# Kernel tuning notes

Hardware: AMD Instinct MI355X
Metric: run time of the kernel (lower is better)

## Reference

```python
import jax, jax.numpy as jnp
import numpy as np

NUM_ITER = 3  # num_itterations

def squash(s):
    # Faithful to the module's (non-standard) squash: out = |s|^2 * s / (1 + |s|^2 * (|s| + 1e-9)).
    # torch sums over dim=-2 of [..., D, 1]; here s is [..., D] so sum over last axis.
    sq = jnp.sum(s * s, axis=-1, keepdims=True)
    norm = jnp.sqrt(sq)
    return sq * s / (1.0 + sq * (norm + 1e-9))

def setup_inputs() -> dict:
    key = jax.random.key(0)
    k1, k2 = jax.random.split(key)
    B, P, N, T, D = 512, 1152, 10, 16, 8
    x = jax.random.normal(k1, (B, P, D), dtype=jnp.float32)          # input capsules
    W = jax.random.normal(k2, (P, N, T, D), dtype=jnp.float32)       # routing transform (torch W with leading 1 dropped)
    return {"x": x, "W": W}

def reference(x, B_unused=None, *, _=None, **__):
    raise RuntimeError('placeholder')

def reference(x, W):
    # prediction u_hat[b,p,n,:] = W[p,n] @ x[b,p]  -> [B, P, N, T]
    pred = jnp.einsum('pntd,bpd->bpnt', W, x)
    B, P, N = pred.shape[0], pred.shape[1], pred.shape[2]
    b_ij = jnp.zeros((B, P, N), dtype=x.dtype)
    v = None
    for i in range(NUM_ITER):
        # torch.tensor(c_ij) detaches the coupling coefficients from the graph
        c = jax.lax.stop_gradient(jax.nn.softmax(b_ij, axis=2))      # softmax over next-caps dim
        s = jnp.einsum('bpn,bpnt->bnt', c, pred)                     # weighted sum over prev caps
        v = squash(s)                                                # [B, N, T]
        if i < NUM_ITER - 1:
            a = jnp.einsum('bpnt,bnt->bpn', pred, v)                 # agreement
            b_ij = b_ij + jnp.mean(a, axis=0, keepdims=True)         # torch mean over batch, keepdim, broadcast-add
    return v[..., None]  # [B, numNextCaps, nextCapsDim, 1] matching torch v_j.squeeze(1)
```

## Files before the change

kernel.cpp:

```cpp
#include <hip/hip_runtime.h>
#include <hip/hip_bf16.h>


typedef __attribute__((ext_vector_type(8))) short bfrag;
typedef __attribute__((ext_vector_type(4))) float f32x4;

constexpr int B_ = 512, P_ = 1152, N_ = 10, NT_ = 160;
constexpr int K1_ = 9216, NKC_ = 288;

__device__ __forceinline__ unsigned short f2bf(float f) {
    unsigned u = __float_as_uint(f);
    return (unsigned short)((u + 0x7fffu + ((u >> 16) & 1u)) >> 16);
}
__device__ __forceinline__ float bf2f(unsigned short s) {
    return __uint_as_float((unsigned)s << 16);
}
__device__ __forceinline__ bfrag mkfrag(f32x4 a, f32x4 b, float c) {
    bfrag f;
    f[0] = (short)f2bf(a.x * c); f[1] = (short)f2bf(a.y * c);
    f[2] = (short)f2bf(a.z * c); f[3] = (short)f2bf(a.w * c);
    f[4] = (short)f2bf(b.x * c); f[5] = (short)f2bf(b.y * c);
    f[6] = (short)f2bf(b.z * c); f[7] = (short)f2bf(b.w * c);
    return f;
}

__global__ __launch_bounds__(256) void k_prep(const float* __restrict__ x,
                                              const float* __restrict__ W,
                                              unsigned short* __restrict__ Xb,
                                              unsigned short* __restrict__ Xga,
                                              unsigned short* __restrict__ Wc,
                                              unsigned short* __restrict__ Wb) {
    const int bid = blockIdx.x, tid = threadIdx.x;
    const int w = tid >> 6, ln = tid & 63, col = ln & 15, q = ln >> 4;
    if (bid < 1152) {
        __shared__ unsigned short tile[64][72];
        const int pd0 = (bid >> 3) * 64, b0 = (bid & 7) * 64;
        const int c0 = tid & 63, r0 = tid >> 6;
#pragma unroll
        for (int i = 0; i < 16; ++i) {
            const int br = i * 4 + r0;
            tile[c0][br] = f2bf(x[(size_t)(b0 + br) * K1_ + pd0 + c0]);
        }
        __syncthreads();
#pragma unroll
        for (int fi = 0; fi < 2; ++fi) {
            const int f = w + fi * 4;
            const int pdblk_l = f & 3, kc_l = f >> 2;
            bfrag fr;
#pragma unroll
            for (int j = 0; j < 8; ++j)
                fr[j] = (short)tile[pdblk_l * 16 + col][kc_l * 32 + q * 8 + j];
            const size_t addr = ((size_t)(((pd0 >> 4) + pdblk_l) * 16 + (b0 >> 5) + kc_l)) * 512 + ln * 8;
            *(bfrag*)(Xga + addr) = fr;
        }
#pragma unroll
        for (int fi = 0; fi < 2; ++fi) {
            const int f = w + fi * 4;
            const int mblk_l = f & 3, kc_l = f >> 2;
            bfrag fr;
#pragma unroll
            for (int j = 0; j < 8; ++j)
                fr[j] = (short)tile[kc_l * 32 + q * 8 + j][mblk_l * 16 + col];
            const size_t addr = ((size_t)(((b0 >> 4) + mblk_l) * NKC_ + (pd0 >> 5) + kc_l)) * 512 + ln * 8;
            *(bfrag*)(Xb + addr) = fr;
        }
    } else if (bid < 1872) {
        const int task = (bid - 1152) * 4 + w;
        const int n = task / NKC_, kc = task % NKC_;
        const int p = kc * 4 + q;
        const float* wr = W + ((size_t)p * NT_ + n * 16 + col) * 8;
        const bfrag f = mkfrag(*(const f32x4*)wr, *(const f32x4*)(wr + 4), 0.1f);
        *(bfrag*)(Wc + ((size_t)(n * NKC_ + kc)) * 512 + ln * 8) = f;
    } else {
        const int idx = (bid - 1872) * 256 + tid;
        const int p = ((idx >> 6) * 16 + (idx & 15)) >> 3, d = idx & 7;
        const int q2 = (idx & 63) >> 4;
        unsigned short* dst = Wb + (size_t)idx * 40;
#pragma unroll
        for (int mt = 0; mt < N_; ++mt)
#pragma unroll
            for (int r = 0; r < 4; ++r)
                dst[mt * 4 + r] = f2bf(W[((size_t)p * NT_ + mt * 16 + q2 * 4 + r) * 8 + d]);
    }
}

__global__ __launch_bounds__(1024) void k_sv(const unsigned short* __restrict__ Xb,
                                             const unsigned short* __restrict__ Wc,
                                             unsigned short* __restrict__ Vt,
                                             float* __restrict__ outp,
                                             int final_it) {
    __shared__ float red[16][2][256];
    const int tid = threadIdx.x;
    const int w = tid >> 6, lane = tid & 63, col = lane & 15, q = lane >> 4;
    const int mblk = blockIdx.x;
    const int n0 = blockIdx.y * 2;

    f32x4 accA = (f32x4){0.f, 0.f, 0.f, 0.f};
    f32x4 accB = (f32x4){0.f, 0.f, 0.f, 0.f};
    const int kc0 = w * 18;
    const unsigned short* Xp = Xb + ((size_t)(mblk * NKC_ + kc0)) * 512 + lane * 8;
    const unsigned short* W0 = Wc + ((size_t)(n0 * NKC_ + kc0)) * 512 + lane * 8;
    const unsigned short* W1 = W0 + (size_t)NKC_ * 512;
#pragma unroll 3
    for (int i = 0; i < 18; ++i) {
        const bfrag a  = *(const bfrag*)Xp;
        const bfrag b0 = *(const bfrag*)W0;
        const bfrag b1 = *(const bfrag*)W1;
        accA = __builtin_amdgcn_mfma_f32_16x16x32_bf16(a, b0, accA, 0, 0, 0);
        accB = __builtin_amdgcn_mfma_f32_16x16x32_bf16(a, b1, accB, 0, 0, 0);
        Xp += 512; W0 += 512; W1 += 512;
    }
#pragma unroll
    for (int r = 0; r < 4; ++r) {
        red[w][0][r * 64 + q * 16 + col] = accA[r];
        red[w][1][r * 64 + q * 16 + col] = accB[r];
    }
    __syncthreads();
    if (w < 2) {
        const int mt = n0 + w;
#pragma unroll
        for (int r = 0; r < 4; ++r) {
            const int li = r * 64 + q * 16 + col;
            float s = 0.f;
#pragma unroll
            for (int j = 0; j < 16; ++j) s += red[j][w][li];
            float sq = s * s;
            sq += __shfl_xor(sq, 1);
            sq += __shfl_xor(sq, 2);
            sq += __shfl_xor(sq, 4);
            sq += __shfl_xor(sq, 8);
            const float norm = sqrtf(sq);
            const float scale = sq / (1.0f + sq * (norm + 1e-9f));
            const float vv = s * scale;
            const int b = mblk * 16 + q * 4 + r;
            if (final_it) {
                outp[(size_t)b * NT_ + mt * 16 + col] = vv;
            } else {
                const int b5 = b & 31;
                Vt[((size_t)((mblk >> 1) * N_ + mt)) * 512
                   + ((b5 >> 3) * 16 + col) * 8 + (b5 & 7)] = f2bf(vv);
            }
        }
    }
}

__global__ __launch_bounds__(512) void k_ga(const unsigned short* __restrict__ Vt,
                                            const unsigned short* __restrict__ Xga,
                                            const unsigned short* __restrict__ Wb,
                                            const float* __restrict__ W,
                                            float* __restrict__ bbar,
                                            unsigned short* __restrict__ Wc,
                                            int accum) {
    __shared__ float bred[2][3][64][41];
    __shared__ float csm[4][N_];
    const int tid = threadIdx.x;
    const int w = tid >> 6, lane = tid & 63, col = lane & 15, q = lane >> 4;
    const int half = w >> 2, wl = w & 3;
    const int pdblk = blockIdx.x * 2 + half;
    const int p = (pdblk * 16 + col) >> 3, d = col & 7;

    f32x4 acc[N_];
#pragma unroll
    for (int mt = 0; mt < N_; ++mt) acc[mt] = (f32x4){0.f, 0.f, 0.f, 0.f};

    const int kb0 = wl * 4;
#pragma unroll
    for (int kc = kb0; kc < kb0 + 4; ++kc) {
        const bfrag bf = *(const bfrag*)(Xga + ((size_t)(pdblk * 16 + kc)) * 512 + lane * 8);
#pragma unroll
        for (int mt = 0; mt < N_; ++mt) {
            const bfrag af = *(const bfrag*)(Vt + ((size_t)(kc * N_ + mt)) * 512 + lane * 8);
            acc[mt] = __builtin_amdgcn_mfma_f32_16x16x32_bf16(af, bf, acc[mt], 0, 0, 0);
        }
    }
    if (wl) {
#pragma unroll
        for (int mt = 0; mt < N_; ++mt)
#pragma unroll
            for (int r = 0; r < 4; ++r)
                bred[half][wl - 1][lane][mt * 4 + r] = acc[mt][r];
    }
    __syncthreads();
    if (wl == 0) {
        unsigned short wv[40];
        const unsigned short* ws2 = Wb + ((size_t)(pdblk * 64 + lane)) * 40;
#pragma unroll
        for (int v = 0; v < 40; ++v) wv[v] = ws2[v];
        float part[N_];
#pragma unroll
        for (int mt = 0; mt < N_; ++mt) {
            float s = 0.f;
#pragma unroll
            for (int r = 0; r < 4; ++r) {
                const float h = acc[mt][r] + bred[half][0][lane][mt * 4 + r]
                              + bred[half][1][lane][mt * 4 + r]
                              + bred[half][2][lane][mt * 4 + r];
                s = fmaf(bf2f(wv[mt * 4 + r]), h, s);
            }
            s += __shfl_xor(s, 1);
            s += __shfl_xor(s, 2);
            s += __shfl_xor(s, 4);
            s += __shfl_xor(s, 16);
            s += __shfl_xor(s, 32);
            part[mt] = s;
        }
        if (q == 0 && d == 0) {
            const int pl = col >> 3;
            float bv[N_];
#pragma unroll
            for (int mt = 0; mt < N_; ++mt) {
                bv[mt] = part[mt] * (1.0f / 512.0f);
                if (accum) bv[mt] += bbar[(size_t)p * N_ + mt];
                bbar[(size_t)p * N_ + mt] = bv[mt];
            }
            float m = -1e30f;
#pragma unroll
            for (int mt = 0; mt < N_; ++mt) m = fmaxf(m, bv[mt]);
            float sum = 0.f;
#pragma unroll
            for (int mt = 0; mt < N_; ++mt) { bv[mt] = __expf(bv[mt] - m); sum += bv[mt]; }
            const float inv = 1.f / sum;
#pragma unroll
            for (int mt = 0; mt < N_; ++mt) csm[half * 2 + pl][mt] = bv[mt] * inv;
        }
    }
    __syncthreads();
    const int p0 = blockIdx.x * 4;
#pragma unroll
    for (int task = tid; task < 640; task += 512) {
        const int pl = task / 160, rem = task % 160;
        const int n = rem >> 4, cl = rem & 15;
        const int pp = p0 + pl;
        const float c = csm[pl][n];
        const float* wr = W + ((size_t)pp * NT_ + n * 16 + cl) * 8;
        const size_t addr = ((size_t)(n * NKC_ + (pp >> 2))) * 512 + (pp & 3) * 128 + cl * 8;
        *(bfrag*)(Wc + addr) = mkfrag(*(const f32x4*)wr, *(const f32x4*)(wr + 4), c);
    }
}

extern "C" void kernel_launch(void* const* d_in, const int* in_sizes, int n_in,
                              void* d_out, int out_size, void* d_ws, size_t ws_size,
                              hipStream_t stream) {
    const float* x = (const float*)d_in[0];
    const float* W = (const float*)d_in[1];

    char* wsp = (char*)d_ws;
    float* bbar = (float*)wsp;
    unsigned short* Xb  = (unsigned short*)(wsp + 46080);
    unsigned short* Xga = Xb + (size_t)32 * NKC_ * 512;
    unsigned short* Wc  = Xga + (size_t)576 * 16 * 512;
    unsigned short* Wb  = Wc + (size_t)N_ * NKC_ * 512;
    unsigned short* Vt  = Wb + (size_t)576 * 64 * 40;
    float* outp = (float*)d_out;

    k_prep<<<dim3(2016), dim3(256), 0, stream>>>(x, W, Xb, Xga, Wc, Wb);
    k_sv<<<dim3(32, 5), dim3(1024), 0, stream>>>(Xb, Wc, Vt, outp, 0);
    k_ga<<<dim3(288), dim3(512), 0, stream>>>(Vt, Xga, Wb, W, bbar, Wc, 0);
    k_sv<<<dim3(32, 5), dim3(1024), 0, stream>>>(Xb, Wc, Vt, outp, 0);
    k_ga<<<dim3(288), dim3(512), 0, stream>>>(Vt, Xga, Wb, W, bbar, Wc, 1);
    k_sv<<<dim3(32, 5), dim3(1024), 0, stream>>>(Xb, Wc, Vt, outp, 1);
}
```

Baseline: 136.1 us.

## Register-tile k_sv over two batch tiles and widen k_ga blocks to 1024 threads

```diff
diff --git a/kernel.cpp b/kernel.cpp
--- a/kernel.cpp
+++ b/kernel.cpp
@@ -89,35 +89,45 @@
                                              unsigned short* __restrict__ Vt,
                                              float* __restrict__ outp,
                                              int final_it) {
-    __shared__ float red[16][2][256];
+    __shared__ float red[16][4][256];
     const int tid = threadIdx.x;
     const int w = tid >> 6, lane = tid & 63, col = lane & 15, q = lane >> 4;
-    const int mblk = blockIdx.x;
+    const int bx = blockIdx.x;
     const int n0 = blockIdx.y * 2;
 
-    f32x4 accA = (f32x4){0.f, 0.f, 0.f, 0.f};
-    f32x4 accB = (f32x4){0.f, 0.f, 0.f, 0.f};
+    f32x4 acc00 = (f32x4){0.f, 0.f, 0.f, 0.f};
+    f32x4 acc01 = (f32x4){0.f, 0.f, 0.f, 0.f};
+    f32x4 acc10 = (f32x4){0.f, 0.f, 0.f, 0.f};
+    f32x4 acc11 = (f32x4){0.f, 0.f, 0.f, 0.f};
     const int kc0 = w * 18;
-    const unsigned short* Xp = Xb + ((size_t)(mblk * NKC_ + kc0)) * 512 + lane * 8;
+    const unsigned short* X0 = Xb + ((size_t)((2 * bx) * NKC_ + kc0)) * 512 + lane * 8;
+    const unsigned short* X1 = X0 + (size_t)NKC_ * 512;
     const unsigned short* W0 = Wc + ((size_t)(n0 * NKC_ + kc0)) * 512 + lane * 8;
     const unsigned short* W1 = W0 + (size_t)NKC_ * 512;
 #pragma unroll 3
     for (int i = 0; i < 18; ++i) {
-        const bfrag a  = *(const bfrag*)Xp;
+        const bfrag a0 = *(const bfrag*)X0;
+        const bfrag a1 = *(const bfrag*)X1;
         const bfrag b0 = *(const bfrag*)W0;
         const bfrag b1 = *(const bfrag*)W1;
-        accA = __builtin_amdgcn_mfma_f32_16x16x32_bf16(a, b0, accA, 0, 0, 0);
-        accB = __builtin_amdgcn_mfma_f32_16x16x32_bf16(a, b1, accB, 0, 0, 0);
-        Xp += 512; W0 += 512; W1 += 512;
+        acc00 = __builtin_amdgcn_mfma_f32_16x16x32_bf16(a0, b0, acc00, 0, 0, 0);
+        acc01 = __builtin_amdgcn_mfma_f32_16x16x32_bf16(a0, b1, acc01, 0, 0, 0);
+        acc10 = __builtin_amdgcn_mfma_f32_16x16x32_bf16(a1, b0, acc10, 0, 0, 0);
+        acc11 = __builtin_amdgcn_mfma_f32_16x16x32_bf16(a1, b1, acc11, 0, 0, 0);
+        X0 += 512; X1 += 512; W0 += 512; W1 += 512;
     }
 #pragma unroll
     for (int r = 0; r < 4; ++r) {
-        red[w][0][r * 64 + q * 16 + col] = accA[r];
-        red[w][1][r * 64 + q * 16 + col] = accB[r];
+        const int li = r * 64 + q * 16 + col;
+        red[w][0][li] = acc00[r];
+        red[w][1][li] = acc01[r];
+        red[w][2][li] = acc10[r];
+        red[w][3][li] = acc11[r];
     }
     __syncthreads();
-    if (w < 2) {
-        const int mt = n0 + w;
+    if (w < 4) {
+        const int mi = w >> 1, ni = w & 1;
+        const int mt = n0 + ni;
 #pragma unroll
         for (int r = 0; r < 4; ++r) {
             const int li = r * 64 + q * 16 + col;
@@ -132,31 +142,31 @@
             const float norm = sqrtf(sq);
             const float scale = sq / (1.0f + sq * (norm + 1e-9f));
             const float vv = s * scale;
-            const int b = mblk * 16 + q * 4 + r;
+            const int b = (2 * bx + mi) * 16 + q * 4 + r;
             if (final_it) {
                 outp[(size_t)b * NT_ + mt * 16 + col] = vv;
             } else {
                 const int b5 = b & 31;
-                Vt[((size_t)((mblk >> 1) * N_ + mt)) * 512
+                Vt[((size_t)(bx * N_ + mt)) * 512
                    + ((b5 >> 3) * 16 + col) * 8 + (b5 & 7)] = f2bf(vv);
             }
         }
     }
 }
 
-__global__ __launch_bounds__(512) void k_ga(const unsigned short* __restrict__ Vt,
-                                            const unsigned short* __restrict__ Xga,
-                                            const unsigned short* __restrict__ Wb,
-                                            const float* __restrict__ W,
-                                            float* __restrict__ bbar,
-                                            unsigned short* __restrict__ Wc,
-                                            int accum) {
-    __shared__ float bred[2][3][64][41];
-    __shared__ float csm[4][N_];
+__global__ __launch_bounds__(1024) void k_ga(const unsigned short* __restrict__ Vt,
+                                             const unsigned short* __restrict__ Xga,
+                                             const unsigned short* __restrict__ Wb,
+                                             const float* __restrict__ W,
+                                             float* __restrict__ bbar,
+                                             unsigned short* __restrict__ Wc,
+                                             int accum) {
+    __shared__ float bred[4][3][64][41];
+    __shared__ float csm[8][N_];
     const int tid = threadIdx.x;
     const int w = tid >> 6, lane = tid & 63, col = lane & 15, q = lane >> 4;
-    const int half = w >> 2, wl = w & 3;
-    const int pdblk = blockIdx.x * 2 + half;
+    const int qt = w >> 2, wl = w & 3;
+    const int pdblk = blockIdx.x * 4 + qt;
     const int p = (pdblk * 16 + col) >> 3, d = col & 7;
 
     f32x4 acc[N_];
@@ -178,7 +188,7 @@
         for (int mt = 0; mt < N_; ++mt)
 #pragma unroll
             for (int r = 0; r < 4; ++r)
-                bred[half][wl - 1][lane][mt * 4 + r] = acc[mt][r];
+                bred[qt][wl - 1][lane][mt * 4 + r] = acc[mt][r];
     }
     __syncthreads();
     if (wl == 0) {
@@ -192,9 +202,9 @@
             float s = 0.f;
 #pragma unroll
             for (int r = 0; r < 4; ++r) {
-                const float h = acc[mt][r] + bred[half][0][lane][mt * 4 + r]
-                              + bred[half][1][lane][mt * 4 + r]
-                              + bred[half][2][lane][mt * 4 + r];
+                const float h = acc[mt][r] + bred[qt][0][lane][mt * 4 + r]
+                              + bred[qt][1][lane][mt * 4 + r]
+                              + bred[qt][2][lane][mt * 4 + r];
                 s = fmaf(bf2f(wv[mt * 4 + r]), h, s);
             }
             s += __shfl_xor(s, 1);
@@ -221,13 +231,13 @@
             for (int mt = 0; mt < N_; ++mt) { bv[mt] = __expf(bv[mt] - m); sum += bv[mt]; }
             const float inv = 1.f / sum;
 #pragma unroll
-            for (int mt = 0; mt < N_; ++mt) csm[half * 2 + pl][mt] = bv[mt] * inv;
+            for (int mt = 0; mt < N_; ++mt) csm[qt * 2 + pl][mt] = bv[mt] * inv;
         }
     }
     __syncthreads();
-    const int p0 = blockIdx.x * 4;
-#pragma unroll
-    for (int task = tid; task < 640; task += 512) {
+    const int p0 = blockIdx.x * 8;
+#pragma unroll
+    for (int task = tid; task < 1280; task += 1024) {
         const int pl = task / 160, rem = task % 160;
         const int n = rem >> 4, cl = rem & 15;
         const int pp = p0 + pl;
@@ -254,9 +264,9 @@
     float* outp = (float*)d_out;
 
     k_prep<<<dim3(2016), dim3(256), 0, stream>>>(x, W, Xb, Xga, Wc, Wb);
-    k_sv<<<dim3(32, 5), dim3(1024), 0, stream>>>(Xb, Wc, Vt, outp, 0);
-    k_ga<<<dim3(288), dim3(512), 0, stream>>>(Vt, Xga, Wb, W, bbar, Wc, 0);
-    k_sv<<<dim3(32, 5), dim3(1024), 0, stream>>>(Xb, Wc, Vt, outp, 0);
-    k_ga<<<dim3(288), dim3(512), 0, stream>>>(Vt, Xga, Wb, W, bbar, Wc, 1);
-    k_sv<<<dim3(32, 5), dim3(1024), 0, stream>>>(Xb, Wc, Vt, outp, 1);
-}
+    k_sv<<<dim3(16, 5), dim3(1024), 0, stream>>>(Xb, Wc, Vt, outp, 0);
+    k_ga<<<dim3(144), dim3(1024), 0, stream>>>(Vt, Xga, Wb, W, bbar, Wc, 0);
+    k_sv<<<dim3(16, 5), dim3(1024), 0, stream>>>(Xb, Wc, Vt, outp, 0);
+    k_ga<<<dim3(144), dim3(1024), 0, stream>>>(Vt, Xga, Wb, W, bbar, Wc, 1);
+    k_sv<<<dim3(16, 5), dim3(1024), 0, stream>>>(Xb, Wc, Vt, outp, 1);
+}
```

Result: slower. 146.1 us (+7.3%).

## Stage W through shared memory in prep and widen k_ga blocks to three pd-blocks

Applied to the files above, without the earlier changes.

```diff
diff --git a/kernel.cpp b/kernel.cpp
--- a/kernel.cpp
+++ b/kernel.cpp
@@ -30,11 +30,43 @@
                                               unsigned short* __restrict__ Xga,
                                               unsigned short* __restrict__ Wc,
                                               unsigned short* __restrict__ Wb) {
+    __shared__ float smem[5760];
     const int bid = blockIdx.x, tid = threadIdx.x;
     const int w = tid >> 6, ln = tid & 63, col = ln & 15, q = ln >> 4;
-    if (bid < 1152) {
-        __shared__ unsigned short tile[64][72];
-        const int pd0 = (bid >> 3) * 64, b0 = (bid & 7) * 64;
+    if (bid < 288) {
+        const int pb = bid;
+        const int p0 = pb * 4;
+#pragma unroll
+        for (int k = 0; k < 20; ++k) {
+            const int e = k * 256 + tid;
+            const int pl = e / 1280, rem = e % 1280;
+            const int row = rem >> 3, d = rem & 7;
+            smem[pl * 1440 + row * 9 + d] = W[(size_t)p0 * 1280 + e];
+        }
+        __syncthreads();
+        for (int n = w; n < N_; n += 4) {
+            const float* src = smem + q * 1440 + (n * 16 + col) * 9;
+            bfrag f;
+#pragma unroll
+            for (int j = 0; j < 8; ++j) f[j] = (short)f2bf(src[j] * 0.1f);
+            *(bfrag*)(Wc + ((size_t)(n * NKC_ + pb)) * 512 + ln * 8) = f;
+        }
+        if (tid < 128) {
+            const int pdblk_l = tid >> 6;
+            const int lane = tid & 63, c2 = lane & 15, q2 = lane >> 4;
+            const int p_l = (pdblk_l * 16 + c2) >> 3, d = c2 & 7;
+            const float* src = smem + p_l * 1440 + d;
+            unsigned short* dst = Wb + ((size_t)((2 * pb + pdblk_l) * 64 + lane)) * 40;
+#pragma unroll
+            for (int mt = 0; mt < N_; ++mt)
+#pragma unroll
+                for (int r = 0; r < 4; ++r)
+                    dst[mt * 4 + r] = f2bf(src[(mt * 16 + q2 * 4 + r) * 9]);
+        }
+    } else {
+        unsigned short (*tile)[72] = (unsigned short (*)[72])smem;
+        const int tb = bid - 288;
+        const int pd0 = (tb >> 3) * 64, b0 = (tb & 7) * 64;
         const int c0 = tid & 63, r0 = tid >> 6;
 #pragma unroll
         for (int i = 0; i < 16; ++i) {
@@ -64,23 +96,6 @@
             const size_t addr = ((size_t)(((b0 >> 4) + mblk_l) * NKC_ + (pd0 >> 5) + kc_l)) * 512 + ln * 8;
             *(bfrag*)(Xb + addr) = fr;
         }
-    } else if (bid < 1872) {
-        const int task = (bid - 1152) * 4 + w;
-        const int n = task / NKC_, kc = task % NKC_;
-        const int p = kc * 4 + q;
-        const float* wr = W + ((size_t)p * NT_ + n * 16 + col) * 8;
-        const bfrag f = mkfrag(*(const f32x4*)wr, *(const f32x4*)(wr + 4), 0.1f);
-        *(bfrag*)(Wc + ((size_t)(n * NKC_ + kc)) * 512 + ln * 8) = f;
-    } else {
-        const int idx = (bid - 1872) * 256 + tid;
-        const int p = ((idx >> 6) * 16 + (idx & 15)) >> 3, d = idx & 7;
-        const int q2 = (idx & 63) >> 4;
-        unsigned short* dst = Wb + (size_t)idx * 40;
-#pragma unroll
-        for (int mt = 0; mt < N_; ++mt)
-#pragma unroll
-            for (int r = 0; r < 4; ++r)
-                dst[mt * 4 + r] = f2bf(W[((size_t)p * NT_ + mt * 16 + q2 * 4 + r) * 8 + d]);
     }
 }
 
@@ -144,19 +159,19 @@
     }
 }
 
-__global__ __launch_bounds__(512) void k_ga(const unsigned short* __restrict__ Vt,
+__global__ __launch_bounds__(768) void k_ga(const unsigned short* __restrict__ Vt,
                                             const unsigned short* __restrict__ Xga,
                                             const unsigned short* __restrict__ Wb,
                                             const float* __restrict__ W,
                                             float* __restrict__ bbar,
                                             unsigned short* __restrict__ Wc,
                                             int accum) {
-    __shared__ float bred[2][3][64][41];
-    __shared__ float csm[4][N_];
+    __shared__ float bred[3][3][64][41];
+    __shared__ float csm[6][N_];
     const int tid = threadIdx.x;
     const int w = tid >> 6, lane = tid & 63, col = lane & 15, q = lane >> 4;
-    const int half = w >> 2, wl = w & 3;
-    const int pdblk = blockIdx.x * 2 + half;
+    const int third = w >> 2, wl = w & 3;
+    const int pdblk = blockIdx.x * 3 + third;
     const int p = (pdblk * 16 + col) >> 3, d = col & 7;
 
     f32x4 acc[N_];
@@ -178,7 +193,7 @@
         for (int mt = 0; mt < N_; ++mt)
 #pragma unroll
             for (int r = 0; r < 4; ++r)
-                bred[half][wl - 1][lane][mt * 4 + r] = acc[mt][r];
+                bred[third][wl - 1][lane][mt * 4 + r] = acc[mt][r];
     }
     __syncthreads();
     if (wl == 0) {
@@ -192,9 +207,9 @@
             float s = 0.f;
 #pragma unroll
             for (int r = 0; r < 4; ++r) {
-                const float h = acc[mt][r] + bred[half][0][lane][mt * 4 + r]
-                              + bred[half][1][lane][mt * 4 + r]
-                              + bred[half][2][lane][mt * 4 + r];
+                const float h = acc[mt][r] + bred[third][0][lane][mt * 4 + r]
+                              + bred[third][1][lane][mt * 4 + r]
+                              + bred[third][2][lane][mt * 4 + r];
                 s = fmaf(bf2f(wv[mt * 4 + r]), h, s);
             }
             s += __shfl_xor(s, 1);
@@ -221,13 +236,13 @@
             for (int mt = 0; mt < N_; ++mt) { bv[mt] = __expf(bv[mt] - m); sum += bv[mt]; }
             const float inv = 1.f / sum;
 #pragma unroll
-            for (int mt = 0; mt < N_; ++mt) csm[half * 2 + pl][mt] = bv[mt] * inv;
+            for (int mt = 0; mt < N_; ++mt) csm[third * 2 + pl][mt] = bv[mt] * inv;
         }
     }
     __syncthreads();
-    const int p0 = blockIdx.x * 4;
-#pragma unroll
-    for (int task = tid; task < 640; task += 512) {
+    const int p0 = blockIdx.x * 6;
+#pragma unroll
+    for (int task = tid; task < 960; task += 768) {
         const int pl = task / 160, rem = task % 160;
         const int n = rem >> 4, cl = rem & 15;
         const int pp = p0 + pl;
@@ -253,10 +268,10 @@
     unsigned short* Vt  = Wb + (size_t)576 * 64 * 40;
     float* outp = (float*)d_out;
 
-    k_prep<<<dim3(2016), dim3(256), 0, stream>>>(x, W, Xb, Xga, Wc, Wb);
+    k_prep<<<dim3(1440), dim3(256), 0, stream>>>(x, W, Xb, Xga, Wc, Wb);
     k_sv<<<dim3(32, 5), dim3(1024), 0, stream>>>(Xb, Wc, Vt, outp, 0);
-    k_ga<<<dim3(288), dim3(512), 0, stream>>>(Vt, Xga, Wb, W, bbar, Wc, 0);
+    k_ga<<<dim3(192), dim3(768), 0, stream>>>(Vt, Xga, Wb, W, bbar, Wc, 0);
     k_sv<<<dim3(32, 5), dim3(1024), 0, stream>>>(Xb, Wc, Vt, outp, 0);
-    k_ga<<<dim3(288), dim3(512), 0, stream>>>(Vt, Xga, Wb, W, bbar, Wc, 1);
+    k_ga<<<dim3(192), dim3(768), 0, stream>>>(Vt, Xga, Wb, W, bbar, Wc, 1);
     k_sv<<<dim3(32, 5), dim3(1024), 0, stream>>>(Xb, Wc, Vt, outp, 1);
 }
```

Measured after the change: 133.4 us. 1.02x faster.
